# Kernel optimization log

Hardware: AMD Instinct MI355X
Metric: run time of the kernel (lower is better)

## Reference

```python
import jax, jax.numpy as jnp
import numpy as np

N_HEADS = 16

def setup_inputs() -> dict:
    key = jax.random.key(0)
    k1, k2 = jax.random.split(key)
    qkv = jax.random.normal(k1, (4, 3072, 2048), dtype=jnp.float32)
    encoder_kv = jax.random.normal(k2, (4, 2048, 256), dtype=jnp.float32)
    return {"qkv": qkv, "encoder_kv": encoder_kv}

def reference(qkv, encoder_kv):
    bs, width, length = qkv.shape
    ch = width // (3 * N_HEADS)  # 64
    # [bs*H, 3*ch, T] -> q, k, v each [bs*H, ch, T]
    q, k, v = jnp.split(qkv.reshape(bs * N_HEADS, 3 * ch, length), 3, axis=1)
    # encoder kv: [bs, H*2*ch, S] -> ek, ev each [bs*H, ch, S]
    ek, ev = jnp.split(encoder_kv.reshape(bs * N_HEADS, 2 * ch, -1), 2, axis=1)
    k = jnp.concatenate([ek, k], axis=-1)  # [bs*H, ch, S+T]
    v = jnp.concatenate([ev, v], axis=-1)
    scale = ch ** -0.25  # 1/sqrt(sqrt(ch)), applied to both q and k
    weight = jnp.einsum('bct,bcs->bts', q * scale, k * scale)  # [bs*H, T, S+T]
    weight = jax.nn.softmax(weight.astype(jnp.float32), axis=-1).astype(qkv.dtype)
    a = jnp.einsum('bts,bcs->bct', weight, v)  # [bs*H, ch, T]
    return a.reshape(bs, -1, length)
```

## Files before the change

### kernel.cpp

```cpp
#include <hip/hip_runtime.h>
#include <hip/hip_bf16.h>

typedef __attribute__((ext_vector_type(8))) short bf16x8;
typedef __attribute__((ext_vector_type(4))) float f32x4;
typedef __attribute__((ext_vector_type(4))) unsigned u32x4;
typedef __attribute__((ext_vector_type(2))) unsigned u32x2;

#define T_LEN 2048
#define S_ENC 256
#define QSCALE 0.18033688011112042f

#define BARRIER() __syncthreads()

__device__ __forceinline__ float exp2_hw(float x) {
#if __has_builtin(__builtin_amdgcn_exp2f)
  return __builtin_amdgcn_exp2f(x);
#else
  float r;
  asm("v_exp_f32 %0, %1" : "=v"(r) : "v"(x));
  return r;
#endif
}

__device__ __forceinline__ unsigned cvt_pk_bf16(float lo, float hi) {
  unsigned r;
  asm("v_cvt_pk_bf16_f32 %0, %1, %2" : "=v"(r) : "v"(lo), "v"(hi));
  return r;
}

__device__ __forceinline__ short f2bf(float x) {
  union { __hip_bfloat16 b; short s; } u;
  u.b = __float2bfloat16(x);
  return u.s;
}

__device__ __forceinline__ int swz(int row, int col) {
  return row * 64 + (col ^ ((row & 7) << 3));
}

union PU { u32x4 u; bf16x8 b; };

template<int STRIDE>
__device__ __forceinline__ void issue_loads(
    const float* __restrict__ kb, const float* __restrict__ vb, int s0, int tid,
    float (&kr)[8], float (&kr2)[8], f32x4 (&vr)[4]) {
  const int ks = tid & 63;
  const int kc = (tid >> 6) * 8;
  const float* kp = kb + (size_t)kc * STRIDE + (s0 + ks);
  const float* kp2 = kp + (size_t)32 * STRIDE;
#pragma unroll
  for (int r = 0; r < 8; ++r) kr[r] = kp[(size_t)r * STRIDE];
#pragma unroll
  for (int r = 0; r < 8; ++r) kr2[r] = kp2[(size_t)r * STRIDE];
  const int vg = tid & 15;
  const int vc = tid >> 4;
  const float* vp0 = vb + (size_t)vc * STRIDE + (s0 + 4 * vg);
  vr[0] = *(const f32x4*)(vp0);
  vr[1] = *(const f32x4*)(vp0 + (size_t)32 * STRIDE);
  vr[2] = *(const f32x4*)(vp0 + (size_t)16 * STRIDE);
  vr[3] = *(const f32x4*)(vp0 + (size_t)48 * STRIDE);
}

__device__ __forceinline__ void stage_write(
    short* __restrict__ Kt, short* __restrict__ Vt, int tid,
    const float (&kr)[8], const float (&kr2)[8], const f32x4 (&vr)[4]) {
  const int ks = tid & 63;
  const int kc = (tid >> 6) * 8;
  u32x4 kw;
#pragma unroll
  for (int r = 0; r < 4; ++r) kw[r] = cvt_pk_bf16(kr[2 * r], kr[2 * r + 1]);
  *(u32x4*)(Kt + swz(ks, kc)) = kw;
  u32x4 kw2;
#pragma unroll
  for (int r = 0; r < 4; ++r) kw2[r] = cvt_pk_bf16(kr2[2 * r], kr2[2 * r + 1]);
  *(u32x4*)(Kt + swz(ks, kc + 32)) = kw2;

  const int vg = tid & 15;
  const int vc = tid >> 4;
  const int vcol = 32 * (vg >> 3) + 8 * (vg & 3) + 4 * ((vg >> 2) & 1);
  const int vrow[4] = {vc, vc + 32, vc + 16, vc + 48};
#pragma unroll
  for (int i = 0; i < 4; ++i) {
    u32x2 vw;
    vw[0] = cvt_pk_bf16(vr[i][0], vr[i][1]);
    vw[1] = cvt_pk_bf16(vr[i][2], vr[i][3]);
    *(u32x2*)(Vt + swz(vrow[i], vcol)) = vw;
  }
}

__device__ __forceinline__ void compute_tile(
    const short* __restrict__ Kt, const short* __restrict__ Vt,
    const bf16x8 (&qf)[4][2], f32x4 (&o)[4][4], float (&lp)[4], int tid) {
  const int lane = tid & 63;
  const int ln = lane & 15;
  const int lg = lane >> 4;

  bf16x8 kf[4][2];
#pragma unroll
  for (int mt = 0; mt < 4; ++mt) {
    const int row = 16 * mt + ln;
    kf[mt][0] = *(const bf16x8*)(Kt + swz(row, 8 * lg));
    kf[mt][1] = *(const bf16x8*)(Kt + swz(row, 32 + 8 * lg));
  }

  PU pfrag[4][2];
#pragma unroll
  for (int pr = 0; pr < 2; ++pr) {
    f32x4 sacc[2][4];
#pragma unroll
    for (int q2 = 0; q2 < 2; ++q2)
#pragma unroll
      for (int mt = 0; mt < 4; ++mt) sacc[q2][mt] = (f32x4){0.f, 0.f, 0.f, 0.f};

#pragma unroll
    for (int mt = 0; mt < 4; ++mt)
#pragma unroll
      for (int q2 = 0; q2 < 2; ++q2) {
        const int qt = 2 * pr + q2;
        sacc[q2][mt] = __builtin_amdgcn_mfma_f32_16x16x32_bf16(kf[mt][0], qf[qt][0], sacc[q2][mt], 0, 0, 0);
        sacc[q2][mt] = __builtin_amdgcn_mfma_f32_16x16x32_bf16(kf[mt][1], qf[qt][1], sacc[q2][mt], 0, 0, 0);
      }

#pragma unroll
    for (int q2 = 0; q2 < 2; ++q2) {
      const int qt = 2 * pr + q2;
      float pmt[4];
#pragma unroll
      for (int mt = 0; mt < 4; ++mt) {
        float p0 = exp2_hw(sacc[q2][mt][0]);
        float p1 = exp2_hw(sacc[q2][mt][1]);
        float p2 = exp2_hw(sacc[q2][mt][2]);
        float p3 = exp2_hw(sacc[q2][mt][3]);
        pfrag[qt][mt >> 1].u[2 * (mt & 1) + 0] = cvt_pk_bf16(p0, p1);
        pfrag[qt][mt >> 1].u[2 * (mt & 1) + 1] = cvt_pk_bf16(p2, p3);
        pmt[mt] = (p0 + p1) + (p2 + p3);
      }
      lp[qt] += (pmt[0] + pmt[1]) + (pmt[2] + pmt[3]);
    }
  }

#pragma unroll
  for (int sub = 0; sub < 2; ++sub)
#pragma unroll
    for (int ct = 0; ct < 4; ++ct) {
      const bf16x8 vf = *(const bf16x8*)(Vt + swz(16 * ct + ln, 32 * sub + 8 * lg));
#pragma unroll
      for (int qt = 0; qt < 4; ++qt)
        o[qt][ct] = __builtin_amdgcn_mfma_f32_16x16x32_bf16(vf, pfrag[qt][sub].b, o[qt][ct], 0, 0, 0);
    }
}

__global__ __launch_bounds__(256, 2) void attn_kernel(
    const float* __restrict__ qkv, const float* __restrict__ ekv,
    float* __restrict__ out) {
  const int tid = threadIdx.x;
  const int lane = tid & 63;
  const int wave = tid >> 6;
  const int ln = lane & 15;
  const int lg = lane >> 4;

  const int bh = blockIdx.x & 63;
  const int qb = blockIdx.x >> 6;
  const int t0 = qb * 256 + wave * 64;

  const float* qp  = qkv + (size_t)bh * 192 * T_LEN;
  const float* kp  = qp + (size_t)64 * T_LEN;
  const float* vp  = qp + (size_t)128 * T_LEN;
  const float* ekp = ekv + (size_t)bh * 128 * S_ENC;
  const float* evp = ekp + (size_t)64 * S_ENC;

  __shared__ __attribute__((aligned(16))) short Kt[2][64 * 64];
  __shared__ __attribute__((aligned(16))) short Vt[2][64 * 64];

  bf16x8 qf[4][2];
#pragma unroll
  for (int qt = 0; qt < 4; ++qt)
#pragma unroll
    for (int kk = 0; kk < 2; ++kk)
#pragma unroll
      for (int j = 0; j < 8; ++j)
        qf[qt][kk][j] =
            f2bf(qp[(size_t)(32 * kk + 8 * lg + j) * T_LEN + (t0 + 16 * qt + ln)] * QSCALE);

  f32x4 o[4][4];
#pragma unroll
  for (int qt = 0; qt < 4; ++qt)
#pragma unroll
    for (int ct = 0; ct < 4; ++ct) o[qt][ct] = (f32x4){0.f, 0.f, 0.f, 0.f};
  float lp[4] = {0.f, 0.f, 0.f, 0.f};

  for (int st = 0; st < 4; ++st) {
    float kr[8], kr2[8];
    f32x4 vr[4];
    issue_loads<S_ENC>(ekp, evp, 64 * st, tid, kr, kr2, vr);
    BARRIER();
    stage_write(&Kt[0][0], &Vt[0][0], tid, kr, kr2, vr);
    BARRIER();
    compute_tile(&Kt[0][0], &Vt[0][0], qf, o, lp, tid);
  }

  {
    float kr[8], kr2[8];
    f32x4 vr[4];
    issue_loads<T_LEN>(kp, vp, 0, tid, kr, kr2, vr);
    BARRIER();
    stage_write(&Kt[0][0], &Vt[0][0], tid, kr, kr2, vr);
    issue_loads<T_LEN>(kp, vp, 64, tid, kr, kr2, vr);
    BARRIER();

    int cur = 0;
#pragma unroll 1
    for (int t = 0; t < 31; ++t) {
      stage_write(&Kt[cur ^ 1][0], &Vt[cur ^ 1][0], tid, kr, kr2, vr);
      if (t < 30)
        issue_loads<T_LEN>(kp, vp, 64 * (t + 2), tid, kr, kr2, vr);
      compute_tile(&Kt[cur][0], &Vt[cur][0], qf, o, lp, tid);
      BARRIER();
      cur ^= 1;
    }
    compute_tile(&Kt[cur][0], &Vt[cur][0], qf, o, lp, tid);
  }

#pragma unroll
  for (int qt = 0; qt < 4; ++qt) {
    float l = lp[qt];
    l += __shfl_xor(l, 16);
    l += __shfl_xor(l, 32);
    const float inv = 1.0f / l;
    float* ob = out + (size_t)bh * 64 * T_LEN + (t0 + 16 * qt + ln);
#pragma unroll
    for (int ct = 0; ct < 4; ++ct)
#pragma unroll
      for (int r = 0; r < 4; ++r)
        ob[(size_t)(16 * ct + 4 * lg + r) * T_LEN] = o[qt][ct][r] * inv;
  }
}

extern "C" void kernel_launch(void* const* d_in, const int* in_sizes, int n_in,
                              void* d_out, int out_size, void* d_ws, size_t ws_size,
                              hipStream_t stream) {
  const float* qkv = (const float*)d_in[0];
  const float* ekv = (const float*)d_in[1];
  float* out = (float*)d_out;
  attn_kernel<<<dim3(512), dim3(256), 0, stream>>>(qkv, ekv, out);
}
```

Baseline: 98.77 us.

## Split key sequence across two wave groups per block and reduce partial outputs

The block grows to 512 threads: two groups of 4 waves each handle half of the key/value sequence (encoder and self parts) for the same query rows, and the partial outputs and row sums are combined through shared memory at the end. This doubles the waves available per CU to hide latency with the same grid. In exchange, the double-buffered pipelined K/V load loop is replaced with a simple single-buffer load-barrier-compute loop, and an extra reduction pass through LDS with several barriers is added.

```diff
diff --git a/kernel.cpp b/kernel.cpp
--- a/kernel.cpp
+++ b/kernel.cpp
@@ -9,7 +9,6 @@
 #define T_LEN 2048
 #define S_ENC 256
 #define QSCALE 0.18033688011112042f
-
 #define BARRIER() __syncthreads()
 
 __device__ __forceinline__ float exp2_hw(float x) {
@@ -42,18 +41,18 @@
 
 template<int STRIDE>
 __device__ __forceinline__ void issue_loads(
-    const float* __restrict__ kb, const float* __restrict__ vb, int s0, int tid,
+    const float* __restrict__ kb, const float* __restrict__ vb, int s0, int htid,
     float (&kr)[8], float (&kr2)[8], f32x4 (&vr)[4]) {
-  const int ks = tid & 63;
-  const int kc = (tid >> 6) * 8;
+  const int ks = htid & 63;
+  const int kc = (htid >> 6) * 8;
   const float* kp = kb + (size_t)kc * STRIDE + (s0 + ks);
   const float* kp2 = kp + (size_t)32 * STRIDE;
 #pragma unroll
   for (int r = 0; r < 8; ++r) kr[r] = kp[(size_t)r * STRIDE];
 #pragma unroll
   for (int r = 0; r < 8; ++r) kr2[r] = kp2[(size_t)r * STRIDE];
-  const int vg = tid & 15;
-  const int vc = tid >> 4;
+  const int vg = htid & 15;
+  const int vc = htid >> 4;
   const float* vp0 = vb + (size_t)vc * STRIDE + (s0 + 4 * vg);
   vr[0] = *(const f32x4*)(vp0);
   vr[1] = *(const f32x4*)(vp0 + (size_t)32 * STRIDE);
@@ -62,10 +61,10 @@
 }
 
 __device__ __forceinline__ void stage_write(
-    short* __restrict__ Kt, short* __restrict__ Vt, int tid,
+    short* __restrict__ Kt, short* __restrict__ Vt, int htid,
     const float (&kr)[8], const float (&kr2)[8], const f32x4 (&vr)[4]) {
-  const int ks = tid & 63;
-  const int kc = (tid >> 6) * 8;
+  const int ks = htid & 63;
+  const int kc = (htid >> 6) * 8;
   u32x4 kw;
 #pragma unroll
   for (int r = 0; r < 4; ++r) kw[r] = cvt_pk_bf16(kr[2 * r], kr[2 * r + 1]);
@@ -75,8 +74,8 @@
   for (int r = 0; r < 4; ++r) kw2[r] = cvt_pk_bf16(kr2[2 * r], kr2[2 * r + 1]);
   *(u32x4*)(Kt + swz(ks, kc + 32)) = kw2;
 
-  const int vg = tid & 15;
-  const int vc = tid >> 4;
+  const int vg = htid & 15;
+  const int vc = htid >> 4;
   const int vcol = 32 * (vg >> 3) + 8 * (vg & 3) + 4 * ((vg >> 2) & 1);
   const int vrow[4] = {vc, vc + 32, vc + 16, vc + 48};
 #pragma unroll
@@ -90,8 +89,7 @@
 
 __device__ __forceinline__ void compute_tile(
     const short* __restrict__ Kt, const short* __restrict__ Vt,
-    const bf16x8 (&qf)[4][2], f32x4 (&o)[4][4], float (&lp)[4], int tid) {
-  const int lane = tid & 63;
+    const bf16x8 (&qf)[4][2], f32x4 (&o)[4][4], float (&lp)[4], int lane) {
   const int ln = lane & 15;
   const int lg = lane >> 4;
 
@@ -150,27 +148,32 @@
     }
 }
 
-__global__ __launch_bounds__(256, 2) void attn_kernel(
+__global__ __launch_bounds__(512, 3) void attn_kernel(
     const float* __restrict__ qkv, const float* __restrict__ ekv,
     float* __restrict__ out) {
   const int tid = threadIdx.x;
   const int lane = tid & 63;
   const int wave = tid >> 6;
+  const int w = wave & 3;
+  const int khalf = wave >> 2;
+  const int htid = tid & 255;
   const int ln = lane & 15;
   const int lg = lane >> 4;
 
   const int bh = blockIdx.x & 63;
   const int qb = blockIdx.x >> 6;
-  const int t0 = qb * 256 + wave * 64;
+  const int t0 = qb * 256 + w * 64;
 
   const float* qp  = qkv + (size_t)bh * 192 * T_LEN;
-  const float* kp  = qp + (size_t)64 * T_LEN;
-  const float* vp  = qp + (size_t)128 * T_LEN;
-  const float* ekp = ekv + (size_t)bh * 128 * S_ENC;
+  const float* kp  = qp + (size_t)64 * T_LEN + khalf * 1024;
+  const float* vp  = qp + (size_t)128 * T_LEN + khalf * 1024;
+  const float* ekp = ekv + (size_t)bh * 128 * S_ENC + khalf * 128;
   const float* evp = ekp + (size_t)64 * S_ENC;
 
-  __shared__ __attribute__((aligned(16))) short Kt[2][64 * 64];
-  __shared__ __attribute__((aligned(16))) short Vt[2][64 * 64];
+  __shared__ __attribute__((aligned(16))) short smem[16384];
+  __shared__ float lbuf[4][4][16];
+  short* Kt = smem + khalf * 4096;
+  short* Vt = smem + 8192 + khalf * 4096;
 
   bf16x8 qf[4][2];
 #pragma unroll
@@ -189,50 +192,70 @@
     for (int ct = 0; ct < 4; ++ct) o[qt][ct] = (f32x4){0.f, 0.f, 0.f, 0.f};
   float lp[4] = {0.f, 0.f, 0.f, 0.f};
 
-  for (int st = 0; st < 4; ++st) {
+  for (int st = 0; st < 2; ++st) {
     float kr[8], kr2[8];
     f32x4 vr[4];
-    issue_loads<S_ENC>(ekp, evp, 64 * st, tid, kr, kr2, vr);
-    BARRIER();
-    stage_write(&Kt[0][0], &Vt[0][0], tid, kr, kr2, vr);
-    BARRIER();
-    compute_tile(&Kt[0][0], &Vt[0][0], qf, o, lp, tid);
-  }
-
-  {
+    issue_loads<S_ENC>(ekp, evp, 64 * st, htid, kr, kr2, vr);
+    BARRIER();
+    stage_write(Kt, Vt, htid, kr, kr2, vr);
+    BARRIER();
+    compute_tile(Kt, Vt, qf, o, lp, lane);
+  }
+  for (int st = 0; st < 16; ++st) {
     float kr[8], kr2[8];
     f32x4 vr[4];
-    issue_loads<T_LEN>(kp, vp, 0, tid, kr, kr2, vr);
-    BARRIER();
-    stage_write(&Kt[0][0], &Vt[0][0], tid, kr, kr2, vr);
-    issue_loads<T_LEN>(kp, vp, 64, tid, kr, kr2, vr);
-    BARRIER();
-
-    int cur = 0;
-#pragma unroll 1
-    for (int t = 0; t < 31; ++t) {
-      stage_write(&Kt[cur ^ 1][0], &Vt[cur ^ 1][0], tid, kr, kr2, vr);
-      if (t < 30)
-        issue_loads<T_LEN>(kp, vp, 64 * (t + 2), tid, kr, kr2, vr);
-      compute_tile(&Kt[cur][0], &Vt[cur][0], qf, o, lp, tid);
-      BARRIER();
-      cur ^= 1;
-    }
-    compute_tile(&Kt[cur][0], &Vt[cur][0], qf, o, lp, tid);
-  }
-
+    issue_loads<T_LEN>(kp, vp, 64 * st, htid, kr, kr2, vr);
+    BARRIER();
+    stage_write(Kt, Vt, htid, kr, kr2, vr);
+    BARRIER();
+    compute_tile(Kt, Vt, qf, o, lp, lane);
+  }
+
+  float lsum[4];
 #pragma unroll
   for (int qt = 0; qt < 4; ++qt) {
     float l = lp[qt];
     l += __shfl_xor(l, 16);
     l += __shfl_xor(l, 32);
-    const float inv = 1.0f / l;
-    float* ob = out + (size_t)bh * 64 * T_LEN + (t0 + 16 * qt + ln);
-#pragma unroll
-    for (int ct = 0; ct < 4; ++ct)
-#pragma unroll
-      for (int r = 0; r < 4; ++r)
-        ob[(size_t)(16 * ct + 4 * lg + r) * T_LEN] = o[qt][ct][r] * inv;
+    lsum[qt] = l;
+  }
+  BARRIER();
+  if (khalf == 0 && lg == 0) {
+#pragma unroll
+    for (int qt = 0; qt < 4; ++qt) lbuf[w][qt][ln] = lsum[qt];
+  }
+  BARRIER();
+  float inv[4];
+  if (khalf == 1) {
+#pragma unroll
+    for (int qt = 0; qt < 4; ++qt) inv[qt] = 1.0f / (lsum[qt] + lbuf[w][qt][ln]);
+  }
+
+  f32x4* fbuf = (f32x4*)smem;
+  for (int c = 0; c < 2; ++c) {
+    if (khalf == 0) {
+#pragma unroll
+      for (int qtl = 0; qtl < 2; ++qtl)
+#pragma unroll
+        for (int ct = 0; ct < 4; ++ct)
+          fbuf[(((w * 2 + qtl) * 4 + ct) * 4 + lg) * 16 + ln] = o[2 * c + qtl][ct];
+    }
+    BARRIER();
+    if (khalf == 1) {
+#pragma unroll
+      for (int qtl = 0; qtl < 2; ++qtl) {
+        const int qt = 2 * c + qtl;
+        float* ob = out + (size_t)bh * 64 * T_LEN + (t0 + 16 * qt + ln);
+#pragma unroll
+        for (int ct = 0; ct < 4; ++ct) {
+          const f32x4 t = fbuf[(((w * 2 + qtl) * 4 + ct) * 4 + lg) * 16 + ln];
+#pragma unroll
+          for (int r = 0; r < 4; ++r)
+            ob[(size_t)(16 * ct + 4 * lg + r) * T_LEN] = (o[qt][ct][r] + t[r]) * inv[qt];
+        }
+      }
+    }
+    BARRIER();
   }
 }
 
@@ -242,5 +265,5 @@
   const float* qkv = (const float*)d_in[0];
   const float* ekv = (const float*)d_in[1];
   float* out = (float*)d_out;
-  attn_kernel<<<dim3(512), dim3(256), 0, stream>>>(qkv, ekv, out);
-}
+  attn_kernel<<<dim3(512), dim3(512), 0, stream>>>(qkv, ekv, out);
+}
```

Result: slower. 151.4 us (+53.3%).
